# Performance work log

Measured on AMD Instinct MI355X. Metric: run time of the kernel, lower is better.

## Reference

```python
import jax, jax.numpy as jnp
import numpy as np

B, S, D, H = 4, 8192, 256, 8

def setup_inputs() -> dict:
    key = jax.random.key(0)
    ks = jax.random.split(key, 6)
    return {
        "q": jax.random.normal(ks[0], (B, S, D), dtype=jnp.float32),
        "k": jax.random.normal(ks[1], (B, S, D), dtype=jnp.float32),
        "v": jax.random.normal(ks[2], (B, S, D), dtype=jnp.float32),
        "q_weights": jax.random.normal(ks[3], (H, D, D), dtype=jnp.float32),
        "k_weights": jax.random.normal(ks[4], (H, D, D), dtype=jnp.float32),
        "v_weights": jax.random.normal(ks[5], (H, D, D), dtype=jnp.float32),
    }

def reference(q, k, v, q_weights, k_weights, v_weights):
    # Faithful to the original: einsum 'bsd,hio->bhsd' shares no index between
    # the activation and the weight, so it is q[b,s,d] * sum_{i,o} W[h,i,o].
    qs = jax.nn.softmax(jnp.einsum('bsd,hio->bhsd', q, q_weights), axis=-2)  # softmax over s
    ks = jax.nn.softmax(jnp.einsum('bsd,hio->bhsd', k, k_weights), axis=-2)
    vs = jnp.einsum('bsd,hio->bhsd', v, v_weights)
    # 'bhnk,bhmv->bhkv': n and m are independently summed (outer product of seq-sums)
    global_contexts = jnp.einsum('bhnk,bhmv->bhkv', ks, vs)  # [b,h,d,d]
    # 'bhkv,bhsq->bhsv': k and q independently summed
    out = jnp.einsum('bhkv,bhsq->bhsv', global_contexts, qs)  # [b,h,s,d]
    # AdaptiveMaxPool2d((D,1)) on layout 'b s d h': identity over d (d==D), max over heads
    out = jnp.max(out, axis=1)  # [b,s,d]
    return out
```

## Files before the change

### kernel.cpp

```cpp
#include <hip/hip_runtime.h>

#define B 4
#define S 8192
#define D 256
#define H 8
#define NT 128
#define LOG2E 1.4426950408889634f
#define E2(x) __builtin_amdgcn_exp2f(x)

#define WS_WQ    0
#define WS_WV    8
#define WS_QMAX  16
#define WS_QMIN  (WS_QMAX + B*D)
#define WS_CV    (WS_QMIN + B*D)
#define WS_ZACC  (WS_CV + B*D)
#define WS_KC    (WS_ZACC + B*H*D)
#define WS_WP    (WS_KC + B*H*D)
#define WS_P1    (WS_WP + 1024)
#define WS_P2    (WS_P1 + B*NT*D)
#define WS_P3    (WS_P2 + B*NT*D)

__global__ __launch_bounds__(256) void kA(const float* __restrict__ q,
                                          const float* __restrict__ v,
                                          const float* __restrict__ qw,
                                          const float* __restrict__ vw,
                                          float* __restrict__ ws) {
    const int blk = blockIdx.x;
    const int t = threadIdx.x, w = t >> 6, lane = t & 63;

    if (blk >= B * NT) {
        const int i = blk - B * NT;
        const float4* src = (const float4*)(((i >> 7) ? vw : qw)
                              + (size_t)((i >> 4) & 7) * D * D) + (i & 15) * 1024;
        float sm = 0.f;
        #pragma unroll
        for (int j = 0; j < 4; ++j) {
            float4 a4 = src[j * 256 + t];
            sm += (a4.x + a4.y) + (a4.z + a4.w);
        }
        #pragma unroll
        for (int off = 32; off; off >>= 1) sm += __shfl_down(sm, off, 64);
        if (lane == 0) ws[WS_WP + i * 4 + w] = sm;
        return;
    }

    const int b = blk >> 7, tl = blk & (NT - 1);
    const int g = lane >> 4, cl = lane & 15;
    const int cblk = w * 16 + cl;
    const float4* qbase = (const float4*)(q + ((size_t)b * S + tl * 64) * D);
    const float4* vbase = (const float4*)(v + ((size_t)b * S + tl * 64) * D);
    float4 qmx = make_float4(-3.4e38f, -3.4e38f, -3.4e38f, -3.4e38f);
    float4 qmn = make_float4(3.4e38f, 3.4e38f, 3.4e38f, 3.4e38f);
    float4 vs = make_float4(0.f, 0.f, 0.f, 0.f);
    #pragma unroll 4
    for (int i = 0; i < 16; ++i) {
        const int row = i * 4 + g;
        float4 a4 = qbase[row * 64 + cblk];
        qmx.x = fmaxf(qmx.x, a4.x); qmx.y = fmaxf(qmx.y, a4.y);
        qmx.z = fmaxf(qmx.z, a4.z); qmx.w = fmaxf(qmx.w, a4.w);
        qmn.x = fminf(qmn.x, a4.x); qmn.y = fminf(qmn.y, a4.y);
        qmn.z = fminf(qmn.z, a4.z); qmn.w = fminf(qmn.w, a4.w);
        float4 b4 = vbase[row * 64 + cblk];
        vs.x += b4.x; vs.y += b4.y; vs.z += b4.z; vs.w += b4.w;
    }
    #pragma unroll
    for (int off = 16; off <= 32; off <<= 1) {
        qmx.x = fmaxf(qmx.x, __shfl_xor(qmx.x, off, 64));
        qmx.y = fmaxf(qmx.y, __shfl_xor(qmx.y, off, 64));
        qmx.z = fmaxf(qmx.z, __shfl_xor(qmx.z, off, 64));
        qmx.w = fmaxf(qmx.w, __shfl_xor(qmx.w, off, 64));
        qmn.x = fminf(qmn.x, __shfl_xor(qmn.x, off, 64));
        qmn.y = fminf(qmn.y, __shfl_xor(qmn.y, off, 64));
        qmn.z = fminf(qmn.z, __shfl_xor(qmn.z, off, 64));
        qmn.w = fminf(qmn.w, __shfl_xor(qmn.w, off, 64));
        vs.x += __shfl_xor(vs.x, off, 64);
        vs.y += __shfl_xor(vs.y, off, 64);
        vs.z += __shfl_xor(vs.z, off, 64);
        vs.w += __shfl_xor(vs.w, off, 64);
    }
    if (g == 0) {
        size_t pi = (size_t)(b * NT + tl) * D + cblk * 4;
        *(float4*)&ws[WS_P1 + pi] = qmx;
        *(float4*)&ws[WS_P2 + pi] = qmn;
        *(float4*)&ws[WS_P3 + pi] = vs;
    }
}

__global__ __launch_bounds__(256) void kB(float* __restrict__ ws) {
    const int blk = blockIdx.x, t = threadIdx.x;
    if (blk < 32) {
        const int bb = blk >> 3, oct = blk & 7;
        const int dl = t >> 3, sub = t & 7;
        const int d = oct * 32 + dl;
        float mx = -3.4e38f, mn = 3.4e38f, sm = 0.f;
        #pragma unroll 4
        for (int i = 0; i < 16; ++i) {
            size_t idx = (size_t)(bb * NT + sub * 16 + i) * D + d;
            mx = fmaxf(mx, ws[WS_P1 + idx]);
            mn = fminf(mn, ws[WS_P2 + idx]);
            sm += ws[WS_P3 + idx];
        }
        #pragma unroll
        for (int off = 1; off < 8; off <<= 1) {
            mx = fmaxf(mx, __shfl_xor(mx, off, 64));
            mn = fminf(mn, __shfl_xor(mn, off, 64));
            sm += __shfl_xor(sm, off, 64);
        }
        if (sub == 0) {
            ws[WS_QMAX + bb * D + d] = mx;
            ws[WS_QMIN + bb * D + d] = mn;
            ws[WS_CV + bb * D + d] = sm * (float)D;
        }
    } else if (blk == 32) {
        const int o = t >> 4, j = t & 15;
        float s = 0.f;
        #pragma unroll
        for (int ww = 0; ww < 4; ++ww) s += ws[WS_WP + (o * 16 + j) * 4 + ww];
        #pragma unroll
        for (int off = 1; off < 16; off <<= 1) s += __shfl_xor(s, off, 64);
        if (j == 0) ws[(o >= 8) ? (WS_WV + o - 8) : (WS_WQ + o)] = s;
    } else {
        #pragma unroll
        for (int e = 0; e < 8; ++e)
            *(float4*)&ws[WS_ZACC + e * 1024 + t * 4] = make_float4(0.f, 0.f, 0.f, 0.f);
    }
}

__global__ __launch_bounds__(256) void kC(const float* __restrict__ q,
                                          float* __restrict__ ws) {
    const int blk = blockIdx.x;
    const int b = blk >> 8, c = blk & 255;
    const int d = threadIdx.x;
    const float qmx = ws[WS_QMAX + b * D + d];
    const float qmn = ws[WS_QMIN + b * D + d];
    float a[H], cc[H], z[H];
    #pragma unroll
    for (int h = 0; h < H; ++h) {
        float wq_ = ws[WS_WQ + h];
        float M = (wq_ >= 0.f) ? wq_ * qmx : wq_ * qmn;
        a[h] = wq_ * LOG2E;
        cc[h] = -M * LOG2E;
        z[h] = 0.f;
    }
    const float* qp = q + ((size_t)b * S + c * 32) * D + d;
    #pragma unroll 4
    for (int r = 0; r < 32; ++r) {
        float qv = qp[(size_t)r * D];
        #pragma unroll
        for (int h = 0; h < H; ++h) z[h] += E2(fmaf(qv, a[h], cc[h]));
    }
    #pragma unroll
    for (int h = 0; h < H; ++h)
        atomicAdd(&ws[WS_ZACC + (b * H + h) * D + d], z[h]);
}

__global__ __launch_bounds__(256) void kD(float* __restrict__ ws) {
    const int b = blockIdx.x >> 3, h = blockIdx.x & 7;
    const int d = threadIdx.x;
    const float wq_ = ws[WS_WQ + h];
    const float M = (wq_ >= 0.f) ? wq_ * ws[WS_QMAX + b * D + d]
                                 : wq_ * ws[WS_QMIN + b * D + d];
    ws[WS_KC + (b * H + h) * D + d] =
        -M * LOG2E - __builtin_amdgcn_logf(ws[WS_ZACC + (b * H + h) * D + d]);
}

__global__ __launch_bounds__(256) void kE(const float* __restrict__ q,
                                          const float* __restrict__ ws,
                                          float* __restrict__ out) {
    __shared__ float kcs[H * D];
    __shared__ float ab2[16 * 2];

    const int blk = blockIdx.x;
    const int b = blk >> 9, tl = blk & 511;
    const int t = threadIdx.x, w = t >> 6, lane = t & 63;
    const int r = t >> 4, slice = t & 15;

    const float4* qp = (const float4*)(q + ((size_t)b * S + tl * 16 + r) * D
                                       + slice * 16);
    const float4 q0 = qp[0], q1 = qp[1], q2 = qp[2], q3 = qp[3];

    const int dst = ((t >> 2) & 3) * 64 + (t >> 4) * 4 + (t & 3);
    #pragma unroll
    for (int h = 0; h < H; ++h)
        kcs[h * 256 + dst] = ws[WS_KC + (b * H + h) * D + t];

    float a[H], wv_[H];
    #pragma unroll
    for (int h = 0; h < H; ++h) {
        a[h] = ws[WS_WQ + h] * LOG2E;
        wv_[h] = ws[WS_WV + h];
    }
    const float4 cv4 = *(const float4*)&ws[WS_CV + b * D + lane * 4];
    __syncthreads();

    float p[H];
    #pragma unroll
    for (int h = 0; h < H; ++h) p[h] = 0.f;

    const float4* kc4 = (const float4*)kcs;
    #pragma unroll
    for (int j = 0; j < 4; ++j) {
        const float4 qv = (j == 0) ? q0 : (j == 1) ? q1 : (j == 2) ? q2 : q3;
        #pragma unroll
        for (int h = 0; h < H; ++h) {
            const float4 k = kc4[h * 64 + j * 16 + slice];
            p[h] += (E2(fmaf(qv.x, a[h], k.x)) + E2(fmaf(qv.y, a[h], k.y)))
                  + (E2(fmaf(qv.z, a[h], k.z)) + E2(fmaf(qv.w, a[h], k.w)));
        }
    }
    #pragma unroll
    for (int st = 1; st < 16; st <<= 1) {
        #pragma unroll
        for (int h = 0; h < H; ++h) p[h] += __shfl_xor(p[h], st, 16);
    }
    float amax = -3.4e38f, amin = 3.4e38f;
    #pragma unroll
    for (int h = 0; h < H; ++h) {
        const float A = wv_[h] * p[h];
        amax = fmaxf(amax, A);
        amin = fminf(amin, A);
    }
    if (slice == 0) {
        ab2[r * 2] = amax;
        ab2[r * 2 + 1] = amin;
    }
    __syncthreads();

    float* og = out + ((size_t)b * S + tl * 16 + w * 4) * D;
    #pragma unroll
    for (int rr = 0; rr < 4; ++rr) {
        const float am = ab2[(w * 4 + rr) * 2];
        const float an = ab2[(w * 4 + rr) * 2 + 1];
        float4 o;
        o.x = (cv4.x >= 0.f) ? cv4.x * am : cv4.x * an;
        o.y = (cv4.y >= 0.f) ? cv4.y * am : cv4.y * an;
        o.z = (cv4.z >= 0.f) ? cv4.z * am : cv4.z * an;
        o.w = (cv4.w >= 0.f) ? cv4.w * am : cv4.w * an;
        *(float4*)&og[(size_t)rr * D + lane * 4] = o;
    }
}

extern "C" void kernel_launch(void* const* d_in, const int* in_sizes, int n_in,
                              void* d_out, int out_size, void* d_ws, size_t ws_size,
                              hipStream_t stream) {
    const float* q  = (const float*)d_in[0];
    const float* v  = (const float*)d_in[2];
    const float* qw = (const float*)d_in[3];
    const float* vw = (const float*)d_in[5];
    float* out = (float*)d_out;
    float* ws  = (float*)d_ws;

    kA<<<B * NT + 256, 256, 0, stream>>>(q, v, qw, vw, ws);
    kB<<<34, 256, 0, stream>>>(ws);
    kC<<<1024, 256, 0, stream>>>(q, ws);
    kD<<<B * H, 256, 0, stream>>>(ws);
    kE<<<B * 512, 256, 0, stream>>>(q, ws, out);
}
```

Baseline: 61.24 us.

## Use online-softmax chunk merge to drop global q max/min pass and a launch

The global q max/min pass and the atomic Z accumulation are replaced by per-chunk local max/min with per-chunk partition sums, merged later by an online-softmax style rescale in a reduce kernel. This removes one full read of q in the first kernel and cuts the pipeline from five launches to four. Weight-sum reduction is now recomputed inside each block via a shared helper. In exchange it writes larger per-chunk workspace arrays (B*256*H*D partials), and the merge kernel runs a long serial loop over 256 chunks in only 32 blocks.

New measurement: 69.66 us. +13.7%, slower.

```diff
diff --git a/kernel.cpp b/kernel.cpp
--- a/kernel.cpp
+++ b/kernel.cpp
@@ -4,32 +4,39 @@
 #define S 8192
 #define D 256
 #define H 8
-#define NT 128
 #define LOG2E 1.4426950408889634f
 #define E2(x) __builtin_amdgcn_exp2f(x)
 
 #define WS_WQ    0
 #define WS_WV    8
-#define WS_QMAX  16
-#define WS_QMIN  (WS_QMAX + B*D)
-#define WS_CV    (WS_QMIN + B*D)
-#define WS_ZACC  (WS_CV + B*D)
-#define WS_KC    (WS_ZACC + B*H*D)
+#define WS_CV    16
+#define WS_KC    (WS_CV + B*D)
 #define WS_WP    (WS_KC + B*H*D)
-#define WS_P1    (WS_WP + 1024)
-#define WS_P2    (WS_P1 + B*NT*D)
-#define WS_P3    (WS_P2 + B*NT*D)
-
-__global__ __launch_bounds__(256) void kA(const float* __restrict__ q,
-                                          const float* __restrict__ v,
+#define WS_P3    (WS_WP + 1024)
+#define WS_QMAXC (WS_P3 + B*128*D)
+#define WS_QMINC (WS_QMAXC + B*256*D)
+#define WS_ZC    (WS_QMINC + B*256*D)
+
+__device__ __forceinline__ void reduce_wp(const float* __restrict__ ws,
+                                          float* wsum, int t) {
+    const int o = t >> 4, j = t & 15;
+    const float* wp = ws + WS_WP + o * 64;
+    float s = (wp[j] + wp[16 + j]) + (wp[32 + j] + wp[48 + j]);
+    #pragma unroll
+    for (int st = 1; st < 16; st <<= 1) s += __shfl_xor(s, st, 16);
+    if (j == 0) wsum[o] = s;
+    __syncthreads();
+}
+
+__global__ __launch_bounds__(256) void kP(const float* __restrict__ v,
                                           const float* __restrict__ qw,
                                           const float* __restrict__ vw,
                                           float* __restrict__ ws) {
     const int blk = blockIdx.x;
     const int t = threadIdx.x, w = t >> 6, lane = t & 63;
 
-    if (blk >= B * NT) {
-        const int i = blk - B * NT;
+    if (blk >= 512) {
+        const int i = blk - 512;
         const float4* src = (const float4*)(((i >> 7) ? vw : qw)
                               + (size_t)((i >> 4) & 7) * D * D) + (i & 15) * 1024;
         float sm = 0.f;
@@ -40,128 +47,106 @@
         }
         #pragma unroll
         for (int off = 32; off; off >>= 1) sm += __shfl_down(sm, off, 64);
-        if (lane == 0) ws[WS_WP + i * 4 + w] = sm;
+        if (lane == 0) ws[WS_WP + (i >> 4) * 64 + (i & 15) * 4 + w] = sm;
         return;
     }
 
-    const int b = blk >> 7, tl = blk & (NT - 1);
+    const int b = blk >> 7, tl = blk & 127;
     const int g = lane >> 4, cl = lane & 15;
     const int cblk = w * 16 + cl;
-    const float4* qbase = (const float4*)(q + ((size_t)b * S + tl * 64) * D);
     const float4* vbase = (const float4*)(v + ((size_t)b * S + tl * 64) * D);
-    float4 qmx = make_float4(-3.4e38f, -3.4e38f, -3.4e38f, -3.4e38f);
-    float4 qmn = make_float4(3.4e38f, 3.4e38f, 3.4e38f, 3.4e38f);
     float4 vs = make_float4(0.f, 0.f, 0.f, 0.f);
     #pragma unroll 4
     for (int i = 0; i < 16; ++i) {
-        const int row = i * 4 + g;
-        float4 a4 = qbase[row * 64 + cblk];
-        qmx.x = fmaxf(qmx.x, a4.x); qmx.y = fmaxf(qmx.y, a4.y);
-        qmx.z = fmaxf(qmx.z, a4.z); qmx.w = fmaxf(qmx.w, a4.w);
-        qmn.x = fminf(qmn.x, a4.x); qmn.y = fminf(qmn.y, a4.y);
-        qmn.z = fminf(qmn.z, a4.z); qmn.w = fminf(qmn.w, a4.w);
-        float4 b4 = vbase[row * 64 + cblk];
+        float4 b4 = vbase[(i * 4 + g) * 64 + cblk];
         vs.x += b4.x; vs.y += b4.y; vs.z += b4.z; vs.w += b4.w;
     }
     #pragma unroll
     for (int off = 16; off <= 32; off <<= 1) {
-        qmx.x = fmaxf(qmx.x, __shfl_xor(qmx.x, off, 64));
-        qmx.y = fmaxf(qmx.y, __shfl_xor(qmx.y, off, 64));
-        qmx.z = fmaxf(qmx.z, __shfl_xor(qmx.z, off, 64));
-        qmx.w = fmaxf(qmx.w, __shfl_xor(qmx.w, off, 64));
-        qmn.x = fminf(qmn.x, __shfl_xor(qmn.x, off, 64));
-        qmn.y = fminf(qmn.y, __shfl_xor(qmn.y, off, 64));
-        qmn.z = fminf(qmn.z, __shfl_xor(qmn.z, off, 64));
-        qmn.w = fminf(qmn.w, __shfl_xor(qmn.w, off, 64));
         vs.x += __shfl_xor(vs.x, off, 64);
         vs.y += __shfl_xor(vs.y, off, 64);
         vs.z += __shfl_xor(vs.z, off, 64);
         vs.w += __shfl_xor(vs.w, off, 64);
     }
-    if (g == 0) {
-        size_t pi = (size_t)(b * NT + tl) * D + cblk * 4;
-        *(float4*)&ws[WS_P1 + pi] = qmx;
-        *(float4*)&ws[WS_P2 + pi] = qmn;
-        *(float4*)&ws[WS_P3 + pi] = vs;
-    }
-}
-
-__global__ __launch_bounds__(256) void kB(float* __restrict__ ws) {
-    const int blk = blockIdx.x, t = threadIdx.x;
-    if (blk < 32) {
-        const int bb = blk >> 3, oct = blk & 7;
-        const int dl = t >> 3, sub = t & 7;
-        const int d = oct * 32 + dl;
-        float mx = -3.4e38f, mn = 3.4e38f, sm = 0.f;
-        #pragma unroll 4
-        for (int i = 0; i < 16; ++i) {
-            size_t idx = (size_t)(bb * NT + sub * 16 + i) * D + d;
-            mx = fmaxf(mx, ws[WS_P1 + idx]);
-            mn = fminf(mn, ws[WS_P2 + idx]);
-            sm += ws[WS_P3 + idx];
-        }
-        #pragma unroll
-        for (int off = 1; off < 8; off <<= 1) {
-            mx = fmaxf(mx, __shfl_xor(mx, off, 64));
-            mn = fminf(mn, __shfl_xor(mn, off, 64));
-            sm += __shfl_xor(sm, off, 64);
-        }
-        if (sub == 0) {
-            ws[WS_QMAX + bb * D + d] = mx;
-            ws[WS_QMIN + bb * D + d] = mn;
-            ws[WS_CV + bb * D + d] = sm * (float)D;
-        }
-    } else if (blk == 32) {
-        const int o = t >> 4, j = t & 15;
-        float s = 0.f;
-        #pragma unroll
-        for (int ww = 0; ww < 4; ++ww) s += ws[WS_WP + (o * 16 + j) * 4 + ww];
-        #pragma unroll
-        for (int off = 1; off < 16; off <<= 1) s += __shfl_xor(s, off, 64);
-        if (j == 0) ws[(o >= 8) ? (WS_WV + o - 8) : (WS_WQ + o)] = s;
-    } else {
-        #pragma unroll
-        for (int e = 0; e < 8; ++e)
-            *(float4*)&ws[WS_ZACC + e * 1024 + t * 4] = make_float4(0.f, 0.f, 0.f, 0.f);
-    }
-}
-
-__global__ __launch_bounds__(256) void kC(const float* __restrict__ q,
+    if (g == 0)
+        *(float4*)&ws[WS_P3 + (size_t)(b * 128 + tl) * D + cblk * 4] = vs;
+}
+
+__global__ __launch_bounds__(256) void kZ(const float* __restrict__ q,
                                           float* __restrict__ ws) {
+    __shared__ float wsum[16];
+    reduce_wp(ws, wsum, threadIdx.x);
+
     const int blk = blockIdx.x;
     const int b = blk >> 8, c = blk & 255;
     const int d = threadIdx.x;
-    const float qmx = ws[WS_QMAX + b * D + d];
-    const float qmn = ws[WS_QMIN + b * D + d];
-    float a[H], cc[H], z[H];
+    const float* qp = q + ((size_t)b * S + (size_t)c * 32) * D + d;
+
+    float qv[32];
+    #pragma unroll
+    for (int r = 0; r < 32; ++r) qv[r] = qp[(size_t)r * D];
+
+    float mx = qv[0], mn = qv[0];
+    #pragma unroll
+    for (int r = 1; r < 32; ++r) {
+        mx = fmaxf(mx, qv[r]);
+        mn = fminf(mn, qv[r]);
+    }
+    ws[WS_QMAXC + (size_t)(b * 256 + c) * D + d] = mx;
+    ws[WS_QMINC + (size_t)(b * 256 + c) * D + d] = mn;
+
+    float A[H], cc[H], z[H];
     #pragma unroll
     for (int h = 0; h < H; ++h) {
-        float wq_ = ws[WS_WQ + h];
-        float M = (wq_ >= 0.f) ? wq_ * qmx : wq_ * qmn;
-        a[h] = wq_ * LOG2E;
-        cc[h] = -M * LOG2E;
+        A[h] = wsum[h] * LOG2E;
+        cc[h] = -((A[h] >= 0.f) ? A[h] * mx : A[h] * mn);
         z[h] = 0.f;
     }
-    const float* qp = q + ((size_t)b * S + c * 32) * D + d;
-    #pragma unroll 4
+    #pragma unroll
     for (int r = 0; r < 32; ++r) {
-        float qv = qp[(size_t)r * D];
-        #pragma unroll
-        for (int h = 0; h < H; ++h) z[h] += E2(fmaf(qv, a[h], cc[h]));
-    }
-    #pragma unroll
-    for (int h = 0; h < H; ++h)
-        atomicAdd(&ws[WS_ZACC + (b * H + h) * D + d], z[h]);
-}
-
-__global__ __launch_bounds__(256) void kD(float* __restrict__ ws) {
-    const int b = blockIdx.x >> 3, h = blockIdx.x & 7;
-    const int d = threadIdx.x;
-    const float wq_ = ws[WS_WQ + h];
-    const float M = (wq_ >= 0.f) ? wq_ * ws[WS_QMAX + b * D + d]
-                                 : wq_ * ws[WS_QMIN + b * D + d];
-    ws[WS_KC + (b * H + h) * D + d] =
-        -M * LOG2E - __builtin_amdgcn_logf(ws[WS_ZACC + (b * H + h) * D + d]);
+        #pragma unroll
+        for (int h = 0; h < H; ++h) z[h] += E2(fmaf(qv[r], A[h], cc[h]));
+    }
+    const size_t zb = WS_ZC + ((size_t)(b * 256 + c) * H) * D + d;
+    #pragma unroll
+    for (int h = 0; h < H; ++h) ws[zb + h * D] = z[h];
+}
+
+__global__ __launch_bounds__(256) void kM(float* __restrict__ ws) {
+    __shared__ float wsum[16];
+    reduce_wp(ws, wsum, threadIdx.x);
+    const int blk = blockIdx.x, t = threadIdx.x;
+
+    if (blk < 32) {
+        const int b = blk >> 3, h = blk & 7;
+        const float A = wsum[h] * LOG2E;
+        float Mrun = -3.4e38f, Zrun = 0.f;
+        #pragma unroll 4
+        for (int c = 0; c < 256; ++c) {
+            const float mxc = ws[WS_QMAXC + (size_t)(b * 256 + c) * D + t];
+            const float mnc = ws[WS_QMINC + (size_t)(b * 256 + c) * D + t];
+            const float zc  = ws[WS_ZC + ((size_t)(b * 256 + c) * H + h) * D + t];
+            const float Mc = (A >= 0.f) ? A * mxc : A * mnc;
+            const float nM = fmaxf(Mrun, Mc);
+            Zrun = Zrun * E2(Mrun - nM) + zc * E2(Mc - nM);
+            Mrun = nM;
+        }
+        ws[WS_KC + (size_t)(b * H + h) * D + t] =
+            -Mrun - __builtin_amdgcn_logf(Zrun);
+    } else if (blk < 64) {
+        const int bb = (blk - 32) >> 3, oct = (blk - 32) & 7;
+        const int dl = t >> 3, sub = t & 7;
+        const int d = oct * 32 + dl;
+        float sm = 0.f;
+        #pragma unroll 4
+        for (int i = 0; i < 16; ++i)
+            sm += ws[WS_P3 + (size_t)(bb * 128 + sub * 16 + i) * D + d];
+        #pragma unroll
+        for (int off = 1; off < 8; off <<= 1) sm += __shfl_xor(sm, off, 64);
+        if (sub == 0) ws[WS_CV + bb * D + d] = sm * (float)D;
+    } else {
+        if (t < 16) ws[(t >= 8) ? (WS_WV + t - 8) : (WS_WQ + t)] = wsum[t];
+    }
 }
 
 __global__ __launch_bounds__(256) void kE(const float* __restrict__ q,
@@ -182,7 +167,7 @@
     const int dst = ((t >> 2) & 3) * 64 + (t >> 4) * 4 + (t & 3);
     #pragma unroll
     for (int h = 0; h < H; ++h)
-        kcs[h * 256 + dst] = ws[WS_KC + (b * H + h) * D + t];
+        kcs[h * 256 + dst] = ws[WS_KC + (size_t)(b * H + h) * D + t];
 
     float a[H], wv_[H];
     #pragma unroll
@@ -250,9 +235,8 @@
     float* out = (float*)d_out;
     float* ws  = (float*)d_ws;
 
-    kA<<<B * NT + 256, 256, 0, stream>>>(q, v, qw, vw, ws);
-    kB<<<34, 256, 0, stream>>>(ws);
-    kC<<<1024, 256, 0, stream>>>(q, ws);
-    kD<<<B * H, 256, 0, stream>>>(ws);
+    kP<<<768, 256, 0, stream>>>(v, qw, vw, ws);
+    kZ<<<B * 256, 256, 0, stream>>>(q, ws);
+    kM<<<65, 256, 0, stream>>>(ws);
     kE<<<B * 512, 256, 0, stream>>>(q, ws, out);
 }
```

## Fold log-normalizer kernel into output kernel and halve partial-sum grid

Applied to the files above, without the earlier changes.

Removes the separate kD launch by computing the per-head log-normalizer constants directly in kE's shared-memory fill from ZACC and the q max/min. kC now processes 64 rows per block with half as many blocks, which halves the atomic traffic. In kE, the second __syncthreads and the LDS staging of row max/min are replaced by wave shuffles, since each wave already holds its own rows, and launch bounds request higher occupancy. The cost is that every kE block recomputes the 2048 log values, which is redundant work on the transcendental unit.

New measurement: 51.69 us, median of 2. 15.6% less time.

```diff
diff --git a/kernel.cpp b/kernel.cpp
--- a/kernel.cpp
+++ b/kernel.cpp
@@ -14,8 +14,7 @@
 #define WS_QMIN  (WS_QMAX + B*D)
 #define WS_CV    (WS_QMIN + B*D)
 #define WS_ZACC  (WS_CV + B*D)
-#define WS_KC    (WS_ZACC + B*H*D)
-#define WS_WP    (WS_KC + B*H*D)
+#define WS_WP    (WS_ZACC + B*H*D)
 #define WS_P1    (WS_WP + 1024)
 #define WS_P2    (WS_P1 + B*NT*D)
 #define WS_P3    (WS_P2 + B*NT*D)
@@ -117,7 +116,7 @@
         #pragma unroll
         for (int ww = 0; ww < 4; ++ww) s += ws[WS_WP + (o * 16 + j) * 4 + ww];
         #pragma unroll
-        for (int off = 1; off < 16; off <<= 1) s += __shfl_xor(s, off, 64);
+        for (int off = 1; off < 16; off <<= 1) s += __shfl_xor(s, off, 16);
         if (j == 0) ws[(o >= 8) ? (WS_WV + o - 8) : (WS_WQ + o)] = s;
     } else {
         #pragma unroll
@@ -129,7 +128,7 @@
 __global__ __launch_bounds__(256) void kC(const float* __restrict__ q,
                                           float* __restrict__ ws) {
     const int blk = blockIdx.x;
-    const int b = blk >> 8, c = blk & 255;
+    const int b = blk >> 7, c = blk & 127;
     const int d = threadIdx.x;
     const float qmx = ws[WS_QMAX + b * D + d];
     const float qmn = ws[WS_QMIN + b * D + d];
@@ -142,33 +141,23 @@
         cc[h] = -M * LOG2E;
         z[h] = 0.f;
     }
-    const float* qp = q + ((size_t)b * S + c * 32) * D + d;
+    const float* qp = q + ((size_t)b * S + c * 64) * D + d;
     #pragma unroll 4
-    for (int r = 0; r < 32; ++r) {
+    for (int r = 0; r < 64; ++r) {
         float qv = qp[(size_t)r * D];
         #pragma unroll
         for (int h = 0; h < H; ++h) z[h] += E2(fmaf(qv, a[h], cc[h]));
     }
     #pragma unroll
     for (int h = 0; h < H; ++h)
-        atomicAdd(&ws[WS_ZACC + (b * H + h) * D + d], z[h]);
-}
-
-__global__ __launch_bounds__(256) void kD(float* __restrict__ ws) {
-    const int b = blockIdx.x >> 3, h = blockIdx.x & 7;
-    const int d = threadIdx.x;
-    const float wq_ = ws[WS_WQ + h];
-    const float M = (wq_ >= 0.f) ? wq_ * ws[WS_QMAX + b * D + d]
-                                 : wq_ * ws[WS_QMIN + b * D + d];
-    ws[WS_KC + (b * H + h) * D + d] =
-        -M * LOG2E - __builtin_amdgcn_logf(ws[WS_ZACC + (b * H + h) * D + d]);
-}
-
-__global__ __launch_bounds__(256) void kE(const float* __restrict__ q,
-                                          const float* __restrict__ ws,
-                                          float* __restrict__ out) {
+        atomicAdd(&ws[WS_ZACC + (size_t)(b * H + h) * D + d], z[h]);
+}
+
+__global__ __launch_bounds__(256, 8) void kE(const float* __restrict__ q,
+                                             const float* __restrict__ ws,
+                                             float* __restrict__ out) {
     __shared__ float kcs[H * D];
-    __shared__ float ab2[16 * 2];
+    __shared__ float wvs[8];
 
     const int blk = blockIdx.x;
     const int b = blk >> 9, tl = blk & 511;
@@ -180,16 +169,18 @@
     const float4 q0 = qp[0], q1 = qp[1], q2 = qp[2], q3 = qp[3];
 
     const int dst = ((t >> 2) & 3) * 64 + (t >> 4) * 4 + (t & 3);
-    #pragma unroll
-    for (int h = 0; h < H; ++h)
-        kcs[h * 256 + dst] = ws[WS_KC + (b * H + h) * D + t];
-
-    float a[H], wv_[H];
+    const float qmx = ws[WS_QMAX + b * D + t];
+    const float qmn = ws[WS_QMIN + b * D + t];
+    float a[H];
     #pragma unroll
     for (int h = 0; h < H; ++h) {
-        a[h] = ws[WS_WQ + h] * LOG2E;
-        wv_[h] = ws[WS_WV + h];
-    }
+        const float wq_ = ws[WS_WQ + h];
+        const float M = (wq_ >= 0.f) ? wq_ * qmx : wq_ * qmn;
+        kcs[h * 256 + dst] = -M * LOG2E
+            - __builtin_amdgcn_logf(ws[WS_ZACC + (size_t)(b * H + h) * D + t]);
+        a[h] = wq_ * LOG2E;
+    }
+    if (t < 8) wvs[t] = ws[WS_WV + t];
     const float4 cv4 = *(const float4*)&ws[WS_CV + b * D + lane * 4];
     __syncthreads();
 
@@ -216,21 +207,16 @@
     float amax = -3.4e38f, amin = 3.4e38f;
     #pragma unroll
     for (int h = 0; h < H; ++h) {
-        const float A = wv_[h] * p[h];
+        const float A = wvs[h] * p[h];
         amax = fmaxf(amax, A);
         amin = fminf(amin, A);
     }
-    if (slice == 0) {
-        ab2[r * 2] = amax;
-        ab2[r * 2 + 1] = amin;
-    }
-    __syncthreads();
 
     float* og = out + ((size_t)b * S + tl * 16 + w * 4) * D;
     #pragma unroll
     for (int rr = 0; rr < 4; ++rr) {
-        const float am = ab2[(w * 4 + rr) * 2];
-        const float an = ab2[(w * 4 + rr) * 2 + 1];
+        const float am = __shfl(amax, rr * 16, 64);
+        const float an = __shfl(amin, rr * 16, 64);
         float4 o;
         o.x = (cv4.x >= 0.f) ? cv4.x * am : cv4.x * an;
         o.y = (cv4.y >= 0.f) ? cv4.y * am : cv4.y * an;
@@ -252,7 +238,6 @@
 
     kA<<<B * NT + 256, 256, 0, stream>>>(q, v, qw, vw, ws);
     kB<<<34, 256, 0, stream>>>(ws);
-    kC<<<1024, 256, 0, stream>>>(q, ws);
-    kD<<<B * H, 256, 0, stream>>>(ws);
+    kC<<<512, 256, 0, stream>>>(q, ws);
     kE<<<B * 512, 256, 0, stream>>>(q, ws, out);
 }
```
